# Kernel optimization log

Measured on AMD Instinct MI355X. Metric: run time of the kernel, lower is better.

The kernel has to match this reference:

```python
import jax, jax.numpy as jnp
import numpy as np

N = 50000      # nodes
E = 800000     # edges (avg degree 16)
G = 50         # graphs in batch (1000 nodes each)
D_IN, H, H2, OUT = 8, 128, 64, 1


def setup_inputs() -> dict:
    key = jax.random.key(0)
    ks = jax.random.split(key, 16)
    src = jax.random.randint(ks[0], (E,), 0, N)
    # every node gets at least one in-edge (forward computes 3/in_deg)
    dst = jnp.concatenate([jnp.arange(N), jax.random.randint(ks[1], (E - N,), 0, N)])
    graph_ids = jnp.arange(N) // (N // G)

    def lin(k, fan_in, fan_out):
        return jax.random.normal(k, (fan_in, fan_out), jnp.float32) / np.float32(np.sqrt(fan_in))

    inp = {"src": src, "dst": dst, "graph_ids": graph_ids}
    dims = [(D_IN, H), (H, H), (H, H), (H, H), (H, H)]
    for i, (fi, fo) in enumerate(dims):
        inp[f"W{i+1}"] = lin(ks[2 + i], fi, fo)
        inp[f"b{i+1}"] = jnp.zeros((fo,), jnp.float32)
    inp["lw1"] = lin(ks[8], H, H2)
    inp["lb1"] = jnp.zeros((H2,), jnp.float32)
    inp["lw2"] = lin(ks[9], H2, OUT)
    inp["lb2"] = jnp.zeros((OUT,), jnp.float32)
    return inp


def reference(src, dst, graph_ids, W1, b1, W2, b2, W3, b3, W4, b4, W5, b5, lw1, lb1, lw2, lb2):
    ones_e = jnp.ones((E,), jnp.float32)
    in_deg = jax.ops.segment_sum(ones_e, dst, num_segments=N)   # [N]
    out_deg = jax.ops.segment_sum(ones_e, src, num_segments=N)  # [N]

    # degree features (8 channels)
    h1 = in_deg[:, None]
    h2 = (in_deg > 3.0).astype(jnp.float32)[:, None]
    h3 = 3.0 / h1
    h4 = (in_deg > 4.0).astype(jnp.float32)[:, None]
    h_ = jnp.concatenate([h1, h2, h3, h4, -h1, -h2, -h3, -h4], axis=1)  # [N,8]

    # DGL GraphConv norm='both': clamp degrees to min 1 for normalization
    norm_src = jnp.maximum(out_deg, 1.0) ** -0.5  # [N]
    norm_dst = jnp.maximum(in_deg, 1.0) ** -0.5   # [N]

    def conv(h, W, b):
        m = (h * norm_src[:, None])[src]                        # [E, d] gather
        agg = jax.ops.segment_sum(m, dst, num_segments=N)       # [N, d] scatter-add
        return agg * norm_dst[:, None] @ W + b

    h_co = jax.nn.relu(conv(h_, W1, b1))
    h_co = jax.nn.relu(conv(h_co, W2, b2))
    h_co = jax.nn.relu(conv(h_co, W3, b3))
    h_co = jax.nn.relu(conv(h_co, W4, b4))
    h_co = jax.nn.relu(conv(h_co, W5, b5))                      # [N, H]

    # dgl.mean_nodes: per-graph mean pool
    counts = jax.ops.segment_sum(jnp.ones((N,), jnp.float32), graph_ids, num_segments=G)
    graph_emb = jax.ops.segment_sum(h_co, graph_ids, num_segments=G) / counts[:, None]  # [G, H]

    # dropout layers are identity in eval mode
    h_emb = jax.nn.relu(graph_emb @ lw1 + lb1)
    pred = jax.nn.sigmoid(h_emb @ lw2 + lb2)                    # [G, 1]
    return (pred, graph_emb, h_co)
```

## Files before the change

kernel.cpp:

```cpp
#include <hip/hip_runtime.h>
#include <math.h>

#define N_NODES 50000
#define N_EDGES 800000
#define N_GRAPHS 50
#define HD 128
#define TM 64
#define POOL_CHUNK 125
#define SCAN_B 256
#define SCAN_NB ((N_NODES + SCAN_B - 1) / SCAN_B)
#define NB_H 128
#define CH_H (N_EDGES / NB_H)
#define NBIN2 (N_NODES / 2)
#define ALDA 132

__global__ __launch_bounds__(256) void k_hist(const int* __restrict__ src,
                                              const int* __restrict__ dst,
                                              unsigned* __restrict__ part_in,
                                              unsigned* __restrict__ part_out) {
    __shared__ unsigned cnt[NBIN2];
    int t = threadIdx.x, b = blockIdx.x;
    int e0 = b * CH_H;
    for (int j = t; j < NBIN2; j += 256) cnt[j] = 0;
    __syncthreads();
    for (int e = e0 + t; e < e0 + CH_H; e += 256) {
        int i = dst[e];
        atomicAdd(&cnt[i >> 1], 1u << ((i & 1) * 16));
    }
    __syncthreads();
    for (int j = t; j < NBIN2; j += 256) part_in[b * NBIN2 + j] = cnt[j];
    __syncthreads();
    for (int j = t; j < NBIN2; j += 256) cnt[j] = 0;
    __syncthreads();
    for (int e = e0 + t; e < e0 + CH_H; e += 256) {
        int i = src[e];
        atomicAdd(&cnt[i >> 1], 1u << ((i & 1) * 16));
    }
    __syncthreads();
    for (int j = t; j < NBIN2; j += 256) part_out[b * NBIN2 + j] = cnt[j];
}

__global__ void k_dreduce(unsigned* __restrict__ part_in,
                          const unsigned* __restrict__ part_out,
                          int* __restrict__ deg_in, int* __restrict__ deg_out) {
    int j = blockIdx.x * blockDim.x + threadIdx.x;
    if (j >= NBIN2) return;
    unsigned run_i = 0, run_o = 0;
    for (int b = 0; b < NB_H; ++b) {
        unsigned pi = part_in[b * NBIN2 + j];
        unsigned po = part_out[b * NBIN2 + j];
        part_in[b * NBIN2 + j] = run_i;
        run_i += pi;
        run_o += po;
    }
    ((int2*)deg_in)[j] = make_int2((int)(run_i & 0xFFFFu), (int)(run_i >> 16));
    ((int2*)deg_out)[j] = make_int2((int)(run_o & 0xFFFFu), (int)(run_o >> 16));
}

__global__ void k_norms(const int* __restrict__ deg_in, const int* __restrict__ deg_out,
                        const int* __restrict__ gids,
                        float* norm_src, float* norm_dst, int* gcount,
                        float4* __restrict__ feat4) {
    __shared__ int hist[N_GRAPHS];
    int t = threadIdx.x;
    if (t < N_GRAPHS) hist[t] = 0;
    __syncthreads();
    int i = blockIdx.x * blockDim.x + t;
    if (i < N_NODES) {
        float di = (float)deg_in[i];
        float dq = (float)deg_out[i];
        float nd = 1.0f / sqrtf(fmaxf(di, 1.0f));
        float ns = 1.0f / sqrtf(fmaxf(dq, 1.0f));
        norm_dst[i] = nd;
        norm_src[i] = ns;
        float4 f;
        f.x = di * ns;
        f.y = (di > 3.0f) ? ns : 0.0f;
        f.z = (3.0f / di) * ns;
        f.w = (di > 4.0f) ? ns : 0.0f;
        feat4[i] = f;
        atomicAdd(&hist[gids[i]], 1);
    }
    __syncthreads();
    if (t < N_GRAPHS && hist[t] != 0) atomicAdd(&gcount[t], hist[t]);
}

__global__ void k_scan1(const int* __restrict__ deg_in, int* off, int* bsum) {
    __shared__ int sh[SCAN_B];
    int t = threadIdx.x;
    int i = blockIdx.x * SCAN_B + t;
    int v = (i < N_NODES) ? deg_in[i] : 0;
    sh[t] = v;
    __syncthreads();
    for (int o = 1; o < SCAN_B; o <<= 1) {
        int u = (t >= o) ? sh[t - o] : 0;
        __syncthreads();
        sh[t] += u;
        __syncthreads();
    }
    if (i < N_NODES) off[i] = sh[t] - v;
    if (t == SCAN_B - 1) bsum[blockIdx.x] = sh[t];
}

__global__ void k_scan2(int* bsum, int* off) {
    __shared__ int sh[SCAN_B];
    int t = threadIdx.x;
    int v = (t < SCAN_NB) ? bsum[t] : 0;
    sh[t] = v;
    __syncthreads();
    for (int o = 1; o < SCAN_B; o <<= 1) {
        int u = (t >= o) ? sh[t - o] : 0;
        __syncthreads();
        sh[t] += u;
        __syncthreads();
    }
    if (t < SCAN_NB) bsum[t] = sh[t] - v;
    if (t == SCAN_B - 1) off[N_NODES] = sh[t];
}

__global__ void k_scan3(int* off, const int* __restrict__ bsum) {
    int b = blockIdx.x, t = threadIdx.x;
    int i = b * SCAN_B + t;
    if (i < N_NODES) off[i] += bsum[b];
}

__global__ __launch_bounds__(256) void k_scatter2(const int* __restrict__ src,
                                                  const int* __restrict__ dst,
                                                  const int* __restrict__ off,
                                                  const unsigned* __restrict__ part_in,
                                                  int* __restrict__ csr) {
    __shared__ unsigned cur[NBIN2];
    int t = threadIdx.x, b = blockIdx.x;
    const unsigned* base = part_in + (size_t)b * NBIN2;
    for (int j = t; j < NBIN2; j += 256) cur[j] = base[j];
    __syncthreads();
    int e0 = b * CH_H;
    for (int e = e0 + t; e < e0 + CH_H; e += 256) {
        int d = dst[e];
        int sh = (d & 1) * 16;
        unsigned old = atomicAdd(&cur[d >> 1], 1u << sh);
        int rank = (int)((old >> sh) & 0xFFFFu);
        csr[off[d] + rank] = src[e];
    }
}

__global__ void k_agg1(const int* __restrict__ off, const int* __restrict__ csr,
                       const float4* __restrict__ feat4,
                       const float* __restrict__ ndst, float* __restrict__ agg8) {
    int i = blockIdx.x * blockDim.x + threadIdx.x;
    if (i >= N_NODES) return;
    int e0 = off[i], e1 = off[i + 1];
    float a0 = 0.f, a1 = 0.f, a2 = 0.f, a3 = 0.f;
    int e = e0;
    for (; e + 1 < e1; e += 2) {
        float4 f0 = feat4[csr[e]];
        float4 f1 = feat4[csr[e + 1]];
        a0 += f0.x + f1.x; a1 += f0.y + f1.y;
        a2 += f0.z + f1.z; a3 += f0.w + f1.w;
    }
    if (e < e1) {
        float4 f0 = feat4[csr[e]];
        a0 += f0.x; a1 += f0.y; a2 += f0.z; a3 += f0.w;
    }
    float nd = ndst[i];
    a0 *= nd; a1 *= nd; a2 *= nd; a3 *= nd;
    float4* p = (float4*)(agg8 + (size_t)i * 8);
    float4 hi = { a0, a1, a2, a3 };
    float4 lo = { -a0, -a1, -a2, -a3 };
    p[0] = hi;
    p[1] = lo;
}

__global__ void k_gemm1(const float* __restrict__ agg8, const float* __restrict__ W,
                        const float* __restrict__ b, const float* __restrict__ nsrc,
                        float* __restrict__ out) {
    __shared__ float Wsh[8 * 128];
    int t = threadIdx.x;
    for (int i = t; i < 1024; i += 256) Wsh[i] = W[i];
    __syncthreads();
    int row = blockIdx.x * 2 + (t >> 7);
    int j = t & 127;
    if (row >= N_NODES) return;
    const float* a = agg8 + (size_t)row * 8;
    float acc = b[j];
#pragma unroll
    for (int k = 0; k < 8; ++k) acc += a[k] * Wsh[k * 128 + j];
    out[(size_t)row * HD + j] = fmaxf(acc, 0.0f) * nsrc[row];
}

__global__ __launch_bounds__(256) void k_agg4(const int* __restrict__ off,
                                              const int* __restrict__ csr,
                                              const float* __restrict__ ndst,
                                              const float* __restrict__ h,
                                              float* __restrict__ out) {
    int wid = (blockIdx.x * blockDim.x + threadIdx.x) >> 6;
    int lane = threadIdx.x & 63;
    if (wid >= N_NODES) return;
    int half = lane >> 5;
    int q = lane & 31;
    int e0 = off[wid], e1 = off[wid + 1];
    float4 a = { 0.f, 0.f, 0.f, 0.f };
    int e = e0 + half;
    for (; e + 6 < e1; e += 8) {
        int s0 = csr[e], s1 = csr[e + 2], s2 = csr[e + 4], s3 = csr[e + 6];
        float4 v0 = *(const float4*)(h + (size_t)s0 * HD + q * 4);
        float4 v1 = *(const float4*)(h + (size_t)s1 * HD + q * 4);
        float4 v2 = *(const float4*)(h + (size_t)s2 * HD + q * 4);
        float4 v3 = *(const float4*)(h + (size_t)s3 * HD + q * 4);
        a.x += v0.x + v1.x + v2.x + v3.x;
        a.y += v0.y + v1.y + v2.y + v3.y;
        a.z += v0.z + v1.z + v2.z + v3.z;
        a.w += v0.w + v1.w + v2.w + v3.w;
    }
    for (; e < e1; e += 2) {
        int s0 = csr[e];
        float4 v0 = *(const float4*)(h + (size_t)s0 * HD + q * 4);
        a.x += v0.x; a.y += v0.y; a.z += v0.z; a.w += v0.w;
    }
    a.x += __shfl_xor(a.x, 32);
    a.y += __shfl_xor(a.y, 32);
    a.z += __shfl_xor(a.z, 32);
    a.w += __shfl_xor(a.w, 32);
    if (half == 0) {
        float nd = ndst[wid];
        a.x *= nd; a.y *= nd; a.z *= nd; a.w *= nd;
        *(float4*)(out + (size_t)wid * HD + q * 4) = a;
    }
}

__global__ void k_agg2(const int* __restrict__ off, const int* __restrict__ csr,
                       const float* __restrict__ ndst,
                       const float* __restrict__ h, float* __restrict__ out) {
    int wid = (blockIdx.x * blockDim.x + threadIdx.x) >> 6;
    int lane = threadIdx.x & 63;
    if (wid >= N_NODES) return;
    int e0 = off[wid], e1 = off[wid + 1];
    float a0 = 0.f, a1 = 0.f;
    int e = e0;
    for (; e + 3 < e1; e += 4) {
        int s0 = csr[e], s1 = csr[e + 1], s2 = csr[e + 2], s3 = csr[e + 3];
        float2 v0 = *(const float2*)(h + (size_t)s0 * HD + lane * 2);
        float2 v1 = *(const float2*)(h + (size_t)s1 * HD + lane * 2);
        float2 v2 = *(const float2*)(h + (size_t)s2 * HD + lane * 2);
        float2 v3 = *(const float2*)(h + (size_t)s3 * HD + lane * 2);
        a0 += v0.x + v1.x + v2.x + v3.x;
        a1 += v0.y + v1.y + v2.y + v3.y;
    }
    for (; e < e1; ++e) {
        int s0 = csr[e];
        float2 v0 = *(const float2*)(h + (size_t)s0 * HD + lane * 2);
        a0 += v0.x; a1 += v0.y;
    }
    float nd = ndst[wid];
    float2 o; o.x = a0 * nd; o.y = a1 * nd;
    *(float2*)(out + (size_t)wid * HD + lane * 2) = o;
}

__global__ __launch_bounds__(256) void k_gemm2(const float* __restrict__ A,
                                               const float* __restrict__ W,
                                               const float* __restrict__ b,
                                               const float* __restrict__ nsrc,
                                               int premult,
                                               float* __restrict__ out) {
    __shared__ float Wsh[128 * 64];
    __shared__ float Ash[64 * ALDA];
    int t = threadIdx.x;
    int row0 = blockIdx.x * TM;
    int jh = blockIdx.y * 64;
    const float4* W4 = (const float4*)W;
#pragma unroll
    for (int i = 0; i < 8; ++i) {
        int idx = t + i * 256;
        int k = idx >> 4;
        int q = idx & 15;
        ((float4*)Wsh)[k * 16 + q] = W4[k * 32 + (jh >> 2) + q];
    }
    const float4* A4 = (const float4*)A;
#pragma unroll
    for (int i = 0; i < 8; ++i) {
        int idx = t + i * 256;
        int r = idx >> 5;
        int q = idx & 31;
        int row = row0 + r;
        if (row >= N_NODES) row = N_NODES - 1;
        float4 v = A4[(size_t)row * 32 + q];
        *(float4*)&Ash[r * ALDA + 4 * q] = v;
    }
    __syncthreads();
    int jq = (t & 15) * 4;
    int r0 = (t >> 4) * 4;
    float4 bv = *(const float4*)(b + jh + jq);
    float acc[4][4];
#pragma unroll
    for (int r = 0; r < 4; ++r) {
        acc[r][0] = bv.x; acc[r][1] = bv.y; acc[r][2] = bv.z; acc[r][3] = bv.w;
    }
#define KSTEP(wv, e0_, e1_, e2_, e3_)                                                   \
    acc[0][0] += e0_ * wv.x; acc[0][1] += e0_ * wv.y; acc[0][2] += e0_ * wv.z; acc[0][3] += e0_ * wv.w; \
    acc[1][0] += e1_ * wv.x; acc[1][1] += e1_ * wv.y; acc[1][2] += e1_ * wv.z; acc[1][3] += e1_ * wv.w; \
    acc[2][0] += e2_ * wv.x; acc[2][1] += e2_ * wv.y; acc[2][2] += e2_ * wv.z; acc[2][3] += e2_ * wv.w; \
    acc[3][0] += e3_ * wv.x; acc[3][1] += e3_ * wv.y; acc[3][2] += e3_ * wv.z; acc[3][3] += e3_ * wv.w;
#pragma unroll 8
    for (int k = 0; k < 128; k += 4) {
        float4 a0 = *(const float4*)&Ash[(r0 + 0) * ALDA + k];
        float4 a1 = *(const float4*)&Ash[(r0 + 1) * ALDA + k];
        float4 a2 = *(const float4*)&Ash[(r0 + 2) * ALDA + k];
        float4 a3 = *(const float4*)&Ash[(r0 + 3) * ALDA + k];
        float4 w0 = *(const float4*)&Wsh[(k + 0) * 64 + jq];
        float4 w1 = *(const float4*)&Wsh[(k + 1) * 64 + jq];
        float4 w2 = *(const float4*)&Wsh[(k + 2) * 64 + jq];
        float4 w3 = *(const float4*)&Wsh[(k + 3) * 64 + jq];
        KSTEP(w0, a0.x, a1.x, a2.x, a3.x)
        KSTEP(w1, a0.y, a1.y, a2.y, a3.y)
        KSTEP(w2, a0.z, a1.z, a2.z, a3.z)
        KSTEP(w3, a0.w, a1.w, a2.w, a3.w)
    }
#undef KSTEP
#pragma unroll
    for (int r = 0; r < 4; ++r) {
        int row = row0 + r0 + r;
        if (row < N_NODES) {
            float sc = premult ? nsrc[row] : 1.0f;
            float* op = out + (size_t)row * HD + jh + jq;
            float2 o01 = { fmaxf(acc[r][0], 0.f) * sc, fmaxf(acc[r][1], 0.f) * sc };
            float2 o23 = { fmaxf(acc[r][2], 0.f) * sc, fmaxf(acc[r][3], 0.f) * sc };
            *(float2*)op = o01;
            *(float2*)(op + 2) = o23;
        }
    }
}

__global__ void k_pool(const float* __restrict__ hco, const int* __restrict__ gids,
                       float* gsum) {
    int f = threadIdx.x;
    int n0 = blockIdx.x * POOL_CHUNK;
    int g = gids[n0];
    float s = 0.f;
    for (int i = 0; i < POOL_CHUNK; ++i)
        s += hco[(size_t)(n0 + i) * HD + f];
    atomicAdd(&gsum[g * HD + f], s);
}

__global__ void k_head(const float* __restrict__ gsum, const int* __restrict__ gcount,
                       const float* __restrict__ lw1, const float* __restrict__ lb1,
                       const float* __restrict__ lw2, const float* __restrict__ lb2,
                       float* __restrict__ dout) {
    __shared__ float ge[128];
    int g = blockIdx.x, j = threadIdx.x;
    float cnt = (float)gcount[g];
    float g0 = gsum[g * HD + j] / cnt;
    float g1 = gsum[g * HD + 64 + j] / cnt;
    ge[j] = g0; ge[64 + j] = g1;
    dout[N_GRAPHS + g * HD + j] = g0;
    dout[N_GRAPHS + g * HD + 64 + j] = g1;
    __syncthreads();
    float acc = lb1[j];
#pragma unroll 4
    for (int k = 0; k < 128; ++k) acc += ge[k] * lw1[k * 64 + j];
    float he = fmaxf(acc, 0.f);
    float p = he * lw2[j];
#pragma unroll
    for (int o = 32; o > 0; o >>= 1) p += __shfl_down(p, o);
    if (j == 0) dout[g] = 1.0f / (1.0f + expf(-(p + lb2[0])));
}

extern "C" void kernel_launch(void* const* d_in, const int* in_sizes, int n_in,
                              void* d_out, int out_size, void* d_ws, size_t ws_size,
                              hipStream_t stream) {
    const int* src  = (const int*)d_in[0];
    const int* dst  = (const int*)d_in[1];
    const int* gids = (const int*)d_in[2];
    const float* W1 = (const float*)d_in[3];  const float* b1 = (const float*)d_in[4];
    const float* W2 = (const float*)d_in[5];  const float* b2 = (const float*)d_in[6];
    const float* W3 = (const float*)d_in[7];  const float* b3 = (const float*)d_in[8];
    const float* W4 = (const float*)d_in[9];  const float* b4 = (const float*)d_in[10];
    const float* W5 = (const float*)d_in[11]; const float* b5 = (const float*)d_in[12];
    const float* lw1 = (const float*)d_in[13]; const float* lb1 = (const float*)d_in[14];
    const float* lw2 = (const float*)d_in[15]; const float* lb2 = (const float*)d_in[16];
    float* out = (float*)d_out;

    char* ws = (char*)d_ws;
    int*    gcount   = (int*)(ws + 0);
    float*  gsum     = (float*)(ws + 256);
    const size_t ZERO_BYTES = 25856;
    int*    deg_in   = (int*)(ws + 26112);
    int*    deg_out  = (int*)(ws + 226304);
    int*    off      = (int*)(ws + 426496);
    int*    csr      = (int*)(ws + 826880);
    float*  norm_src = (float*)(ws + 4026880);
    float*  norm_dst = (float*)(ws + 4227072);
    int*    bsum     = (int*)(ws + 4427264);
    float4* feat4    = (float4*)(ws + 4428288);
    float*  aggbuf   = (float*)(ws + 5228544);
    float*  hws      = (float*)(ws + 30828544);
    const size_t WS_NEEDED = 30828544 + 25600000;

    unsigned* part_in  = (unsigned*)aggbuf;
    unsigned* part_out = (unsigned*)aggbuf + NB_H * NBIN2;

    float* hco = out + (N_GRAPHS + N_GRAPHS * HD);
    bool aligned = (ws_size >= WS_NEEDED);
    float* hbuf = aligned ? hws : hco;

    hipMemsetAsync(ws, 0, ZERO_BYTES, stream);

    k_hist<<<NB_H, 256, 0, stream>>>(src, dst, part_in, part_out);
    k_dreduce<<<(NBIN2 + 255) / 256, 256, 0, stream>>>(part_in, part_out,
                                                       deg_in, deg_out);
    k_norms<<<(N_NODES + 255) / 256, 256, 0, stream>>>(deg_in, deg_out, gids,
                                                       norm_src, norm_dst, gcount, feat4);
    k_scan1<<<SCAN_NB, SCAN_B, 0, stream>>>(deg_in, off, bsum);
    k_scan2<<<1, SCAN_B, 0, stream>>>(bsum, off);
    k_scan3<<<SCAN_NB, SCAN_B, 0, stream>>>(off, bsum);
    k_scatter2<<<NB_H, 256, 0, stream>>>(src, dst, off, part_in, csr);

    k_agg1<<<(N_NODES + 255) / 256, 256, 0, stream>>>(off, csr, feat4, norm_dst, aggbuf);
    k_gemm1<<<N_NODES / 2, 256, 0, stream>>>(aggbuf, W1, b1, norm_src, hbuf);

    const float* Ws[4] = { W2, W3, W4, W5 };
    const float* bs[4] = { b2, b3, b4, b5 };
    dim3 ggrid((N_NODES + TM - 1) / TM, 2);
    for (int L = 0; L < 4; ++L) {
        if (aligned)
            k_agg4<<<(N_NODES * 64 + 255) / 256, 256, 0, stream>>>(off, csr,
                                                                   norm_dst, hbuf, aggbuf);
        else
            k_agg2<<<(N_NODES * 64 + 255) / 256, 256, 0, stream>>>(off, csr,
                                                                   norm_dst, hbuf, aggbuf);
        float* gout = (L < 3) ? hbuf : hco;
        k_gemm2<<<ggrid, 256, 0, stream>>>(aggbuf, Ws[L], bs[L],
                                           norm_src, (L < 3) ? 1 : 0, gout);
    }

    k_pool<<<N_NODES / POOL_CHUNK, 128, 0, stream>>>(hco, gids, gsum);
    k_head<<<N_GRAPHS, 64, 0, stream>>>(gsum, gcount, lw1, lb1, lw2, lb2, out);
}
```

Measured before the change: 551.1 us.

## Split degree histogram across grid, read GEMM A rows directly from global

The degree histogram kernel now builds the in-degree and out-degree histograms in separate blocks along a second grid dimension, rather than running one after the other in the same block. This doubles the histogram parallelism and removes the mid-kernel reset of shared memory. The dense layer kernel drops its shared-memory staging of A tiles: each thread reads its four A rows straight from global memory and the unroll factor drops from 8 to 2. This cuts LDS usage, allowing more blocks per CU, but gives up A reuse across the 16 threads that share each row, so reuse now depends on the cache.

```diff
diff --git a/kernel.cpp b/kernel.cpp
--- a/kernel.cpp
+++ b/kernel.cpp
@@ -12,7 +12,6 @@
 #define NB_H 128
 #define CH_H (N_EDGES / NB_H)
 #define NBIN2 (N_NODES / 2)
-#define ALDA 132
 
 __global__ __launch_bounds__(256) void k_hist(const int* __restrict__ src,
                                               const int* __restrict__ dst,
@@ -20,24 +19,17 @@
                                               unsigned* __restrict__ part_out) {
     __shared__ unsigned cnt[NBIN2];
     int t = threadIdx.x, b = blockIdx.x;
+    const int* idx = blockIdx.y ? src : dst;
+    unsigned* outp = blockIdx.y ? part_out : part_in;
     int e0 = b * CH_H;
     for (int j = t; j < NBIN2; j += 256) cnt[j] = 0;
     __syncthreads();
     for (int e = e0 + t; e < e0 + CH_H; e += 256) {
-        int i = dst[e];
+        int i = idx[e];
         atomicAdd(&cnt[i >> 1], 1u << ((i & 1) * 16));
     }
     __syncthreads();
-    for (int j = t; j < NBIN2; j += 256) part_in[b * NBIN2 + j] = cnt[j];
-    __syncthreads();
-    for (int j = t; j < NBIN2; j += 256) cnt[j] = 0;
-    __syncthreads();
-    for (int e = e0 + t; e < e0 + CH_H; e += 256) {
-        int i = src[e];
-        atomicAdd(&cnt[i >> 1], 1u << ((i & 1) * 16));
-    }
-    __syncthreads();
-    for (int j = t; j < NBIN2; j += 256) part_out[b * NBIN2 + j] = cnt[j];
+    for (int j = t; j < NBIN2; j += 256) outp[b * NBIN2 + j] = cnt[j];
 }
 
 __global__ void k_dreduce(unsigned* __restrict__ part_in,
@@ -256,14 +248,13 @@
     *(float2*)(out + (size_t)wid * HD + lane * 2) = o;
 }
 
-__global__ __launch_bounds__(256) void k_gemm2(const float* __restrict__ A,
+__global__ __launch_bounds__(256) void k_gemm3(const float* __restrict__ A,
                                                const float* __restrict__ W,
                                                const float* __restrict__ b,
                                                const float* __restrict__ nsrc,
                                                int premult,
                                                float* __restrict__ out) {
     __shared__ float Wsh[128 * 64];
-    __shared__ float Ash[64 * ALDA];
     int t = threadIdx.x;
     int row0 = blockIdx.x * TM;
     int jh = blockIdx.y * 64;
@@ -275,20 +266,13 @@
         int q = idx & 15;
         ((float4*)Wsh)[k * 16 + q] = W4[k * 32 + (jh >> 2) + q];
     }
-    const float4* A4 = (const float4*)A;
-#pragma unroll
-    for (int i = 0; i < 8; ++i) {
-        int idx = t + i * 256;
-        int r = idx >> 5;
-        int q = idx & 31;
-        int row = row0 + r;
-        if (row >= N_NODES) row = N_NODES - 1;
-        float4 v = A4[(size_t)row * 32 + q];
-        *(float4*)&Ash[r * ALDA + 4 * q] = v;
-    }
     __syncthreads();
     int jq = (t & 15) * 4;
     int r0 = (t >> 4) * 4;
+    const float* A0 = A + (size_t)min(row0 + r0 + 0, N_NODES - 1) * HD;
+    const float* A1 = A + (size_t)min(row0 + r0 + 1, N_NODES - 1) * HD;
+    const float* A2 = A + (size_t)min(row0 + r0 + 2, N_NODES - 1) * HD;
+    const float* A3 = A + (size_t)min(row0 + r0 + 3, N_NODES - 1) * HD;
     float4 bv = *(const float4*)(b + jh + jq);
     float acc[4][4];
 #pragma unroll
@@ -300,12 +284,12 @@
     acc[1][0] += e1_ * wv.x; acc[1][1] += e1_ * wv.y; acc[1][2] += e1_ * wv.z; acc[1][3] += e1_ * wv.w; \
     acc[2][0] += e2_ * wv.x; acc[2][1] += e2_ * wv.y; acc[2][2] += e2_ * wv.z; acc[2][3] += e2_ * wv.w; \
     acc[3][0] += e3_ * wv.x; acc[3][1] += e3_ * wv.y; acc[3][2] += e3_ * wv.z; acc[3][3] += e3_ * wv.w;
-#pragma unroll 8
+#pragma unroll 2
     for (int k = 0; k < 128; k += 4) {
-        float4 a0 = *(const float4*)&Ash[(r0 + 0) * ALDA + k];
-        float4 a1 = *(const float4*)&Ash[(r0 + 1) * ALDA + k];
-        float4 a2 = *(const float4*)&Ash[(r0 + 2) * ALDA + k];
-        float4 a3 = *(const float4*)&Ash[(r0 + 3) * ALDA + k];
+        float4 a0 = *(const float4*)(A0 + k);
+        float4 a1 = *(const float4*)(A1 + k);
+        float4 a2 = *(const float4*)(A2 + k);
+        float4 a3 = *(const float4*)(A3 + k);
         float4 w0 = *(const float4*)&Wsh[(k + 0) * 64 + jq];
         float4 w1 = *(const float4*)&Wsh[(k + 1) * 64 + jq];
         float4 w2 = *(const float4*)&Wsh[(k + 2) * 64 + jq];
@@ -404,7 +388,7 @@
 
     hipMemsetAsync(ws, 0, ZERO_BYTES, stream);
 
-    k_hist<<<NB_H, 256, 0, stream>>>(src, dst, part_in, part_out);
+    k_hist<<<dim3(NB_H, 2), 256, 0, stream>>>(src, dst, part_in, part_out);
     k_dreduce<<<(NBIN2 + 255) / 256, 256, 0, stream>>>(part_in, part_out,
                                                        deg_in, deg_out);
     k_norms<<<(N_NODES + 255) / 256, 256, 0, stream>>>(deg_in, deg_out, gids,
@@ -428,7 +412,7 @@
             k_agg2<<<(N_NODES * 64 + 255) / 256, 256, 0, stream>>>(off, csr,
                                                                    norm_dst, hbuf, aggbuf);
         float* gout = (L < 3) ? hbuf : hco;
-        k_gemm2<<<ggrid, 256, 0, stream>>>(aggbuf, Ws[L], bs[L],
+        k_gemm3<<<ggrid, 256, 0, stream>>>(aggbuf, Ws[L], bs[L],
                                            norm_src, (L < 3) ? 1 : 0, gout);
     }
 
```

Result: faster. 473.7 us, median of 2 (-14.1%).
